# Optimization experiments

Measured on AMD Instinct MI355X. Metric: run time of the kernel, lower is better.

Reference implementation:

```python
import jax, jax.numpy as jnp
import numpy as np

D_EMBED = 1024
N_HEAD = 16
LEN_TRIM = 1024
LN_EPS = 1e-5


def setup_inputs() -> dict:
    key = jax.random.key(0)
    ks = jax.random.split(key, 8)
    B = 2
    h_q = jax.random.normal(ks[0], (B, LEN_TRIM, D_EMBED), jnp.float32)
    h_kv1 = jax.random.normal(ks[1], (B, LEN_TRIM, D_EMBED), jnp.float32)
    h_kv2 = jax.random.normal(ks[2], (B, 2 * LEN_TRIM, D_EMBED), jnp.float32)
    mask = jax.random.uniform(ks[3], (B, LEN_TRIM, 1), jnp.float32)
    in_proj_w = jax.random.normal(ks[4], (3 * D_EMBED, D_EMBED), jnp.float32) * 0.02
    in_proj_b = jnp.zeros((3 * D_EMBED,), jnp.float32)
    out_w = jax.random.normal(ks[5], (D_EMBED, D_EMBED), jnp.float32) * 0.02
    out_b = jnp.zeros((D_EMBED,), jnp.float32)
    ln_g = jnp.ones((D_EMBED,), jnp.float32)
    ln_b = jnp.zeros((D_EMBED,), jnp.float32)
    return dict(h_q=h_q, h_kv1=h_kv1, h_kv2=h_kv2, mask=mask,
                in_proj_w=in_proj_w, in_proj_b=in_proj_b,
                out_w=out_w, out_b=out_b, ln_g=ln_g, ln_b=ln_b)


def _layernorm(x, g, b):
    mu = jnp.mean(x, axis=-1, keepdims=True)
    var = jnp.mean(jnp.square(x - mu), axis=-1, keepdims=True)
    return (x - mu) * jax.lax.rsqrt(var + LN_EPS) * g + b


def reference(h_q, h_kv1, h_kv2, mask, in_proj_w, in_proj_b, out_w, out_b, ln_g, ln_b):
    B, L, D = h_q.shape
    H = N_HEAD
    dh = D // H
    h_kv = jnp.concatenate((h_kv1, h_kv2), axis=1)  # (B, 3L, D)
    S = h_kv.shape[1]
    Wq, Wk, Wv = jnp.split(in_proj_w, 3, axis=0)
    bq, bk, bv = jnp.split(in_proj_b, 3, axis=0)
    q = (h_q @ Wq.T + bq).reshape(B, L, H, dh).transpose(0, 2, 1, 3)   # (B,H,L,dh)
    k = (h_kv @ Wk.T + bk).reshape(B, S, H, dh).transpose(0, 2, 1, 3)  # (B,H,S,dh)
    v = (h_kv @ Wv.T + bv).reshape(B, S, H, dh).transpose(0, 2, 1, 3)
    scores = jnp.einsum('bhld,bhsd->bhls', q, k) / jnp.sqrt(jnp.float32(dh))
    block = jnp.triu(jnp.ones((L, L), bool), k=1)
    mask_causal = jnp.concatenate((block, block, block), axis=-1)  # (L, S)
    scores = jnp.where(mask_causal, -jnp.inf, scores)
    attn = jax.nn.softmax(scores, axis=-1)
    ctx = jnp.einsum('bhls,bhsd->bhld', attn, v).transpose(0, 2, 1, 3).reshape(B, L, D)
    attn_out = ctx @ out_w.T + out_b
    return _layernorm(h_q + attn_out, ln_g, ln_b) * mask
```

## Files before the change

### kernel.cpp

```cpp
#include <hip/hip_runtime.h>
#include <stdint.h>

typedef unsigned short u16;
typedef unsigned int u32;
typedef __bf16 bf16x8 __attribute__((ext_vector_type(8)));
typedef float floatx4 __attribute__((ext_vector_type(4)));
typedef u16 u16x8 __attribute__((ext_vector_type(8)));
typedef u16 u16x4 __attribute__((ext_vector_type(4)));

__device__ __forceinline__ u16 f2bf(float f) {
    __bf16 h = (__bf16)f;
    return __builtin_bit_cast(u16, h);
}

__device__ __forceinline__ void gll16(const u16* g, u16* l) {
    typedef __attribute__((address_space(1))) u32 gu32;
    typedef __attribute__((address_space(3))) u32 lu32;
    __builtin_amdgcn_global_load_lds((gu32*)g, (lu32*)l, 16, 0, 0);
}

__global__ __launch_bounds__(256) void cvt_all(const float* __restrict__ hq,
                                               const float* __restrict__ kv1,
                                               const float* __restrict__ kv2,
                                               const float* __restrict__ win,
                                               u16* __restrict__ a_q,
                                               u16* __restrict__ a_kv,
                                               u16* __restrict__ wb) {
    const int NQ = 262144, NKV = 786432, NW = 393216;
    int i = blockIdx.x * 256 + threadIdx.x;
    const int stride = gridDim.x * 256;
    for (; i < NQ + NKV + NW; i += stride) {
        const float* src; u16* dst;
        if (i < NQ) {
            src = hq + (long long)i * 8; dst = a_q + (long long)i * 8;
        } else if (i < NQ + NKV) {
            int c = i - NQ;
            int row = c >> 7;
            int col = (c & 127) * 8;
            int b = row >= 3072, r = row - b * 3072;
            src = (r < 1024) ? kv1 + ((long long)(b * 1024 + r)) * 1024 + col
                             : kv2 + ((long long)(b * 2048 + (r - 1024))) * 1024 + col;
            dst = a_kv + (long long)row * 1024 + col;
        } else {
            int c = i - (NQ + NKV);
            src = win + (long long)c * 8; dst = wb + (long long)c * 8;
        }
        floatx4 x = *(const floatx4*)src;
        floatx4 y = *(const floatx4*)(src + 4);
        u16x8 o;
        #pragma unroll
        for (int j = 0; j < 4; j++) { o[j] = f2bf(x[j]); o[4 + j] = f2bf(y[j]); }
        *(u16x8*)dst = o;
    }
}

__global__ __launch_bounds__(256) void cvt_bf16(const float* __restrict__ in,
                                                u16* __restrict__ out, int n8) {
    int i = blockIdx.x * 256 + threadIdx.x;
    const int stride = gridDim.x * 256;
    for (; i < n8; i += stride) {
        floatx4 a = *(const floatx4*)(in + (long long)i * 8);
        floatx4 b = *(const floatx4*)(in + (long long)i * 8 + 4);
        u16x8 o;
        #pragma unroll
        for (int j = 0; j < 4; j++) { o[j] = f2bf(a[j]); o[4 + j] = f2bf(b[j]); }
        *(u16x8*)(out + (long long)i * 8) = o;
    }
}

__global__ __launch_bounds__(256) void gemm_proj(const u16* __restrict__ aq,
                                                 const u16* __restrict__ akv,
                                                 const u16* __restrict__ wb,
                                                 const float* __restrict__ bias,
                                                 u16* __restrict__ Qo,
                                                 u16* __restrict__ Ko,
                                                 u16* __restrict__ VTg) {
    __shared__ u16 lds[2][2][8192];
    const int tid = threadIdx.x;
    const int wave = tid >> 6, lane = tid & 63;
    const int lane16 = lane & 15, quad = lane >> 4;
    const int bid = blockIdx.x;
    const int g = (bid & 7) * 112 + (bid >> 3);
    const bool qblk = g < 128;
    int my, nx;
    if (qblk) { my = g >> 3; nx = g & 7; }
    else { int gg = g - 128; my = gg >> 4; nx = gg & 15; }
    const int rowBase = my * 128;
    const int colBase = nx * 128;
    const int wrow = (qblk ? 0 : 1024) + colBase;
    const int wm = (wave >> 1) * 64, wn = (wave & 1) * 64;

    floatx4 acc[4][4];
    #pragma unroll
    for (int am = 0; am < 4; am++)
        #pragma unroll
        for (int bn = 0; bn < 4; bn++) acc[am][bn] = floatx4{0.f, 0.f, 0.f, 0.f};

    const int srow8 = tid >> 3;
    const int scol = ((tid & 7) ^ (srow8 & 7)) * 8;
    const u16* aS = (qblk ? aq : akv) + (long long)(rowBase + srow8) * 1024 + scol;
    const u16* bS = wb + (long long)(wrow + srow8) * 1024 + scol;
    u16* lbase = &lds[0][0][0];
    const int ldst = wave * 512;

    const int cko0 = ((quad ^ (lane16 & 7)) * 8);
    const int cko1 = (((4 + quad) ^ (lane16 & 7)) * 8);

    {
        u16* dA = lbase; u16* dB = lbase + 8192;
        #pragma unroll
        for (int j = 0; j < 4; j++) {
            gll16(aS + j * 32768, dA + j * 2048 + ldst);
            gll16(bS + j * 32768, dB + j * 2048 + ldst);
        }
    }
    __syncthreads();

    int buf = 0;
    for (int t = 0; t < 16; t++) {
        if (t < 15) {
            const int k0 = (t + 1) * 64;
            u16* dA = lbase + (buf ^ 1) * 16384;
            u16* dB = dA + 8192;
            #pragma unroll
            for (int j = 0; j < 4; j++) {
                gll16(aS + j * 32768 + k0, dA + j * 2048 + ldst);
                gll16(bS + j * 32768 + k0, dB + j * 2048 + ldst);
            }
        }
        const u16* Ab = lbase + buf * 16384;
        const u16* Bb = Ab + 8192;
        u16x8 a0[4], a1[4], b0[4], b1[4];
        #pragma unroll
        for (int i = 0; i < 4; i++) {
            a0[i] = *(const u16x8*)&Ab[(wm + i * 16 + lane16) * 64 + cko0];
            a1[i] = *(const u16x8*)&Ab[(wm + i * 16 + lane16) * 64 + cko1];
            b0[i] = *(const u16x8*)&Bb[(wn + i * 16 + lane16) * 64 + cko0];
            b1[i] = *(const u16x8*)&Bb[(wn + i * 16 + lane16) * 64 + cko1];
        }
        #pragma unroll
        for (int am = 0; am < 4; am++)
            #pragma unroll
            for (int bn = 0; bn < 4; bn++)
                acc[am][bn] = __builtin_amdgcn_mfma_f32_16x16x32_bf16(
                    __builtin_bit_cast(bf16x8, a0[am]),
                    __builtin_bit_cast(bf16x8, b0[bn]), acc[am][bn], 0, 0, 0);
        #pragma unroll
        for (int am = 0; am < 4; am++)
            #pragma unroll
            for (int bn = 0; bn < 4; bn++)
                acc[am][bn] = __builtin_amdgcn_mfma_f32_16x16x32_bf16(
                    __builtin_bit_cast(bf16x8, a1[am]),
                    __builtin_bit_cast(bf16x8, b1[bn]), acc[am][bn], 0, 0, 0);
        __syncthreads();
        buf ^= 1;
    }

    const float* bcol = bias + (qblk ? 0 : 1024) + colBase;
    if (qblk || nx < 8) {
        u16* Cb = qblk ? Qo : Ko;
        #pragma unroll
        for (int am = 0; am < 4; am++)
            #pragma unroll
            for (int bn = 0; bn < 4; bn++)
                #pragma unroll
                for (int r = 0; r < 4; r++) {
                    int row = rowBase + wm + am * 16 + quad * 4 + r;
                    int col = wn + bn * 16 + lane16;
                    float v = acc[am][bn][r] + bcol[col];
                    Cb[(long long)row * 1024 + colBase + col] = f2bf(v);
                }
    } else {
        const int b_ = rowBase >= 3072;
        const int keyBase = rowBase - b_ * 3072 + wm;
        #pragma unroll
        for (int am = 0; am < 4; am++)
            #pragma unroll
            for (int bn = 0; bn < 4; bn++) {
                int col = wn + bn * 16 + lane16;
                int d = colBase - 1024 + col;
                int key0 = keyBase + am * 16 + quad * 4;
                u16x4 pk;
                #pragma unroll
                for (int r = 0; r < 4; r++) pk[r] = f2bf(acc[am][bn][r] + bcol[col]);
                *(u16x4*)&VTg[((long long)(b_ * 1024 + d)) * 3072 + key0] = pk;
            }
    }
}

__global__ __launch_bounds__(256) void gemm_out(const u16* __restrict__ ctx,
                                                const u16* __restrict__ wob,
                                                const float* __restrict__ bias,
                                                float* __restrict__ ao0,
                                                float* __restrict__ ao1) {
    __shared__ u16 lds[2][2][8192];
    const int tid = threadIdx.x;
    const int wave = tid >> 6, lane = tid & 63;
    const int lane16 = lane & 15, quad = lane >> 4;
    const int bid = blockIdx.x;
    const int g = (bid & 7) * 32 + (bid >> 3);
    const int my = g >> 4;
    const int nx = (g & 15) >> 1;
    const int kh = g & 1;
    const int rowBase = my * 128, colBase = nx * 128, kbase = kh * 512;
    const int wm = (wave >> 1) * 64, wn = (wave & 1) * 64;

    floatx4 acc[4][4];
    #pragma unroll
    for (int am = 0; am < 4; am++)
        #pragma unroll
        for (int bn = 0; bn < 4; bn++) acc[am][bn] = floatx4{0.f, 0.f, 0.f, 0.f};

    const int srow8 = tid >> 3;
    const int scol = ((tid & 7) ^ (srow8 & 7)) * 8;
    const u16* aS = ctx + (long long)(rowBase + srow8) * 1024 + kbase + scol;
    const u16* bS = wob + (long long)(colBase + srow8) * 1024 + kbase + scol;
    u16* lbase = &lds[0][0][0];
    const int ldst = wave * 512;
    const int cko0 = ((quad ^ (lane16 & 7)) * 8);
    const int cko1 = (((4 + quad) ^ (lane16 & 7)) * 8);

    {
        u16* dA = lbase; u16* dB = lbase + 8192;
        #pragma unroll
        for (int j = 0; j < 4; j++) {
            gll16(aS + j * 32768, dA + j * 2048 + ldst);
            gll16(bS + j * 32768, dB + j * 2048 + ldst);
        }
    }
    __syncthreads();

    int buf = 0;
    for (int t = 0; t < 8; t++) {
        if (t < 7) {
            const int k0 = (t + 1) * 64;
            u16* dA = lbase + (buf ^ 1) * 16384;
            u16* dB = dA + 8192;
            #pragma unroll
            for (int j = 0; j < 4; j++) {
                gll16(aS + j * 32768 + k0, dA + j * 2048 + ldst);
                gll16(bS + j * 32768 + k0, dB + j * 2048 + ldst);
            }
        }
        const u16* Ab = lbase + buf * 16384;
        const u16* Bb = Ab + 8192;
        u16x8 a0[4], a1[4], b0[4], b1[4];
        #pragma unroll
        for (int i = 0; i < 4; i++) {
            a0[i] = *(const u16x8*)&Ab[(wm + i * 16 + lane16) * 64 + cko0];
            a1[i] = *(const u16x8*)&Ab[(wm + i * 16 + lane16) * 64 + cko1];
            b0[i] = *(const u16x8*)&Bb[(wn + i * 16 + lane16) * 64 + cko0];
            b1[i] = *(const u16x8*)&Bb[(wn + i * 16 + lane16) * 64 + cko1];
        }
        #pragma unroll
        for (int am = 0; am < 4; am++)
            #pragma unroll
            for (int bn = 0; bn < 4; bn++)
                acc[am][bn] = __builtin_amdgcn_mfma_f32_16x16x32_bf16(
                    __builtin_bit_cast(bf16x8, a0[am]),
                    __builtin_bit_cast(bf16x8, b0[bn]), acc[am][bn], 0, 0, 0);
        #pragma unroll
        for (int am = 0; am < 4; am++)
            #pragma unroll
            for (int bn = 0; bn < 4; bn++)
                acc[am][bn] = __builtin_amdgcn_mfma_f32_16x16x32_bf16(
                    __builtin_bit_cast(bf16x8, a1[am]),
                    __builtin_bit_cast(bf16x8, b1[bn]), acc[am][bn], 0, 0, 0);
        __syncthreads();
        buf ^= 1;
    }

    float* Co = kh ? ao1 : ao0;
    #pragma unroll
    for (int am = 0; am < 4; am++)
        #pragma unroll
        for (int bn = 0; bn < 4; bn++)
            #pragma unroll
            for (int r = 0; r < 4; r++) {
                int row = rowBase + wm + am * 16 + quad * 4 + r;
                int col = colBase + wn + bn * 16 + lane16;
                float v = acc[am][bn][r] + (kh == 0 ? bias[col] : 0.f);
                Co[(long long)row * 1024 + col] = v;
            }
}

#define ATTN_TILE(DIAG_, HAVENEXT_)                                           \
{                                                                             \
    const int cur = t & 1;                                                    \
    if (HAVENEXT_) {                                                          \
        const long long ko = (long long)(t + 1) * 65536;                      \
        const long long vo = (long long)(t + 1) * 64;                         \
        _Pragma("unroll")                                                     \
        for (int j = 0; j < 2; j++) {                                         \
            gll16(kS + ko + j * 32768, &Kt[cur ^ 1][j * 2048 + ldst]);        \
            gll16(vS + vo + (long long)j * 32 * 3072, &Vt[cur ^ 1][j * 2048 + ldst]); \
        }                                                                     \
    }                                                                         \
    floatx4 sacc[4];                                                          \
    _Pragma("unroll")                                                         \
    for (int mi = 0; mi < 4; mi++) sacc[mi] = floatx4{0.f, 0.f, 0.f, 0.f};    \
    __builtin_amdgcn_s_setprio(1);                                            \
    _Pragma("unroll")                                                         \
    for (int mi = 0; mi < 4; mi++) {                                          \
        u16x8 kf = *(const u16x8*)&Kt[cur][(mi * 16 + lane16) * 64 + slot0];  \
        sacc[mi] = __builtin_amdgcn_mfma_f32_16x16x32_bf16(                   \
            __builtin_bit_cast(bf16x8, kf), qf[0], sacc[mi], 0, 0, 0);        \
    }                                                                         \
    _Pragma("unroll")                                                         \
    for (int mi = 0; mi < 4; mi++) {                                          \
        u16x8 kf = *(const u16x8*)&Kt[cur][(mi * 16 + lane16) * 64 + slot1];  \
        sacc[mi] = __builtin_amdgcn_mfma_f32_16x16x32_bf16(                   \
            __builtin_bit_cast(bf16x8, kf), qf[1], sacc[mi], 0, 0, 0);        \
    }                                                                         \
    __builtin_amdgcn_s_setprio(0);                                            \
    float tmax = -1e30f;                                                      \
    _Pragma("unroll")                                                         \
    for (int mi = 0; mi < 4; mi++)                                            \
        _Pragma("unroll")                                                     \
        for (int r = 0; r < 4; r++) {                                         \
            float s = sacc[mi][r] * C2;                                       \
            if (DIAG_ && (mi * 16 + quad * 4 + r) > qloc) s = -1e30f;         \
            sacc[mi][r] = s;                                                  \
            tmax = fmaxf(tmax, s);                                            \
        }                                                                     \
    tmax = fmaxf(tmax, __shfl_xor(tmax, 16));                                 \
    tmax = fmaxf(tmax, __shfl_xor(tmax, 32));                                 \
    if (!__all(tmax <= m_i + 8.0f)) {           \
        float m_new = fmaxf(m_i, tmax);                                       \
        float alpha = exp2f(m_i - m_new);                                     \
        _Pragma("unroll")                                                     \
        for (int mi = 0; mi < 4; mi++)                                        \
            _Pragma("unroll")                                                 \
            for (int r = 0; r < 4; r++) o_acc[mi][r] *= alpha;                \
        l_lane *= alpha;                                                      \
        m_i = m_new;                                                          \
    }                                                                         \
    _Pragma("unroll")                                                         \
    for (int mi = 0; mi < 4; mi++) {                                          \
        u16x4 pk;                                                             \
        _Pragma("unroll")                                                     \
        for (int r = 0; r < 4; r++) {                                         \
            float p = exp2f(sacc[mi][r] - m_i);                               \
            l_lane += p;                                                      \
            pk[r] = f2bf(p);                                                  \
        }                                                                     \
        *(u16x4*)&Ps[wave][lane16 * 84 + mi * 16 + quad * 4] = pk;            \
    }                                                                         \
    __builtin_amdgcn_wave_barrier();                                          \
    __builtin_amdgcn_s_setprio(1);                                            \
    _Pragma("unroll")                                                         \
    for (int c = 0; c < 2; c++) {                                             \
        bf16x8 pf = __builtin_bit_cast(bf16x8,                                \
            *(const u16x8*)&Ps[wave][lane16 * 84 + c * 32 + quad * 8]);       \
        const int slot = c ? slot1 : slot0;                                   \
        _Pragma("unroll")                                                     \
        for (int mi = 0; mi < 4; mi++) {                                      \
            bf16x8 vf = __builtin_bit_cast(bf16x8,                            \
                *(const u16x8*)&Vt[cur][(mi * 16 + lane16) * 64 + slot]);     \
            o_acc[mi] = __builtin_amdgcn_mfma_f32_16x16x32_bf16(vf, pf, o_acc[mi], 0, 0, 0); \
        }                                                                     \
    }                                                                         \
    __builtin_amdgcn_s_setprio(0);                                            \
    if (HAVENEXT_) __syncthreads();                                           \
}

__global__ __launch_bounds__(256) void attn_seg(const u16* __restrict__ Q,
                                                const u16* __restrict__ Kb,
                                                const u16* __restrict__ VTg,
                                                float* __restrict__ pO_lo,
                                                float* __restrict__ pO_hi,
                                                float* __restrict__ pml) {
    __shared__ u16 Kt[2][4096];
    __shared__ u16 Vt[2][4096];
    __shared__ u16 Ps[4][1344];
    const int tid = threadIdx.x;
    const int wave = tid >> 6, lane = tid & 63;
    const int lane16 = lane & 15, quad = lane >> 4;
    const int bid = blockIdx.x;
    const int idx_ = (bid & 7) * 192 + (bid >> 3);
    const int qhat = idx_ & 15;
    const int h   = (idx_ >> 4) & 15;
    const int b   = (idx_ >> 8) & 1;
    const int seg = idx_ >> 9;
    const int qt = b ? (15 - qhat) : qhat;
    const int l0 = qt * 64;
    const int wq = wave * 16;
    const float C2 = 0.1803368801f;
    const int qloc = wq + lane16;

    bf16x8 qf[2];
    {
        const u16* qrow = Q + ((long long)(b * 1024 + l0 + wq + lane16)) * 1024 + h * 64;
        qf[0] = __builtin_bit_cast(bf16x8, *(const u16x8*)(qrow + quad * 8));
        qf[1] = __builtin_bit_cast(bf16x8, *(const u16x8*)(qrow + 32 + quad * 8));
    }

    const int srow = tid >> 3;
    const int csw8 = ((tid & 7) ^ (srow & 7)) * 8;
    const long long bh = ((long long)b * 3072) * 1024 + h * 64;
    const u16* kS = Kb + bh + ((long long)(seg * 1024)) * 1024
                    + (long long)srow * 1024 + csw8;
    const u16* vS = VTg + ((long long)(b * 1024 + h * 64 + srow)) * 3072
                    + seg * 1024 + csw8;
    const int ldst = wave * 512;

    {
        #pragma unroll
        for (int j = 0; j < 2; j++) {
            gll16(kS + j * 32768, &Kt[0][j * 2048 + ldst]);
            gll16(vS + (long long)j * 32 * 3072, &Vt[0][j * 2048 + ldst]);
        }
    }
    __syncthreads();

    const int slot0 = ((quad ^ (lane16 & 7)) * 8);
    const int slot1 = (((4 + quad) ^ (lane16 & 7)) * 8);

    float m_i = -1e30f, l_lane = 0.f;
    floatx4 o_acc[4];
    #pragma unroll
    for (int mi = 0; mi < 4; mi++) o_acc[mi] = floatx4{0.f, 0.f, 0.f, 0.f};

    for (int t = 0; t < qt; t++) ATTN_TILE(false, true)
    { int t = qt; ATTN_TILE(true, false) }

    float l_i = l_lane;
    l_i += __shfl_xor(l_i, 16);
    l_i += __shfl_xor(l_i, 32);

    const int p = ((b * 16 + h) * 16 + qt) * 3 + seg;
    float* op = (p < 512) ? (pO_lo + (long long)p * 4096)
                          : (pO_hi + (long long)(p - 512) * 4096);
    if (quad == 0) {
        pml[(long long)p * 128 + (wq + lane16) * 2]     = m_i;
        pml[(long long)p * 128 + (wq + lane16) * 2 + 1] = l_i;
    }
    float* orow = op + (long long)(wq + lane16) * 64;
    #pragma unroll
    for (int mi = 0; mi < 4; mi++)
        *(floatx4*)(orow + mi * 16 + quad * 4) = o_acc[mi];
}

__global__ __launch_bounds__(256) void attn_combine(const float* __restrict__ pO_lo,
                                                    const float* __restrict__ pO_hi,
                                                    const float* __restrict__ pml,
                                                    u16* __restrict__ Ctx) {
    const int g = blockIdx.x;
    const int qt = g & 15;
    const int h  = (g >> 4) & 15;
    const int b  = g >> 8;
    const int t  = threadIdx.x;
    const int q  = t >> 2;
    const int d0 = (t & 3) * 16;
    const int p0 = g * 3;

    float m[3], l[3];
    #pragma unroll
    for (int s = 0; s < 3; s++) {
        m[s] = pml[(long long)(p0 + s) * 128 + q * 2];
        l[s] = pml[(long long)(p0 + s) * 128 + q * 2 + 1];
    }
    float M = fmaxf(m[0], fmaxf(m[1], m[2]));
    float w[3];
    #pragma unroll
    for (int s = 0; s < 3; s++) w[s] = exp2f(m[s] - M);
    float L = w[0] * l[0] + w[1] * l[1] + w[2] * l[2];
    float invL = 1.0f / L;

    const float* O[3];
    #pragma unroll
    for (int s = 0; s < 3; s++) {
        int pp = p0 + s;
        O[s] = ((pp < 512) ? (pO_lo + (long long)pp * 4096)
                           : (pO_hi + (long long)(pp - 512) * 4096))
               + (long long)q * 64 + d0;
    }

    long long crow = ((long long)(b * 1024 + qt * 64 + q)) * 1024 + h * 64 + d0;
    #pragma unroll
    for (int i = 0; i < 16; i += 4) {
        floatx4 a  = *(const floatx4*)(O[0] + i);
        floatx4 bb = *(const floatx4*)(O[1] + i);
        floatx4 cc = *(const floatx4*)(O[2] + i);
        #pragma unroll
        for (int j = 0; j < 4; j++)
            Ctx[crow + i + j] = f2bf((w[0] * a[j] + w[1] * bb[j] + w[2] * cc[j]) * invL);
    }
}

__global__ __launch_bounds__(256) void ln_kernel(const float* __restrict__ AO0,
                                                 const float* __restrict__ AO1,
                                                 const float* __restrict__ HQ,
                                                 const float* __restrict__ g,
                                                 const float* __restrict__ bb,
                                                 const float* __restrict__ mask,
                                                 float* __restrict__ Out) {
    const int row = blockIdx.x;
    const int t = threadIdx.x;
    const int base = row * 1024 + t * 4;
    floatx4 a0 = *(const floatx4*)&AO0[base];
    floatx4 a1 = *(const floatx4*)&AO1[base];
    floatx4 hq = *(const floatx4*)&HQ[base];
    float x[4];
    #pragma unroll
    for (int i = 0; i < 4; i++) x[i] = a0[i] + a1[i] + hq[i];
    float s = x[0] + x[1] + x[2] + x[3];
    float ss = x[0]*x[0] + x[1]*x[1] + x[2]*x[2] + x[3]*x[3];
    #pragma unroll
    for (int off = 32; off >= 1; off >>= 1) { s += __shfl_xor(s, off); ss += __shfl_xor(ss, off); }
    __shared__ float smem[8];
    int wave = t >> 6, lane = t & 63;
    if (lane == 0) { smem[wave] = s; smem[4 + wave] = ss; }
    __syncthreads();
    s  = smem[0] + smem[1] + smem[2] + smem[3];
    ss = smem[4] + smem[5] + smem[6] + smem[7];
    float mu  = s * (1.f / 1024.f);
    float var = ss * (1.f / 1024.f) - mu * mu;
    float rs  = rsqrtf(var + 1e-5f);
    float mv  = mask[row];
    floatx4 g4 = *(const floatx4*)&g[t * 4];
    floatx4 b4 = *(const floatx4*)&bb[t * 4];
    floatx4 y4;
    #pragma unroll
    for (int i = 0; i < 4; i++) y4[i] = ((x[i] - mu) * rs * g4[i] + b4[i]) * mv;
    *(floatx4*)&Out[base] = y4;
}

extern "C" void kernel_launch(void* const* d_in, const int* in_sizes, int n_in,
                              void* d_out, int out_size, void* d_ws, size_t ws_size,
                              hipStream_t stream) {
    (void)in_sizes; (void)n_in; (void)out_size; (void)ws_size;
    const float* h_q   = (const float*)d_in[0];
    const float* h_kv1 = (const float*)d_in[1];
    const float* h_kv2 = (const float*)d_in[2];
    const float* maskp = (const float*)d_in[3];
    const float* win   = (const float*)d_in[4];
    const float* binp  = (const float*)d_in[5];
    const float* wout  = (const float*)d_in[6];
    const float* bout  = (const float*)d_in[7];
    const float* ln_g  = (const float*)d_in[8];
    const float* ln_b  = (const float*)d_in[9];
    float* outp = (float*)d_out;

    char* ws = (char*)d_ws;
    const size_t MB = 1024 * 1024;
    u16*   q_b   = (u16*)(ws);
    u16*   k_b   = (u16*)(ws + 4 * MB);
    u16*   vT    = (u16*)(ws + 16 * MB);
    u16*   ctx_b = q_b;
    u16*   a_q   = (u16*)(ws + 28 * MB);
    u16*   a_kv  = (u16*)(ws + 32 * MB);
    u16*   wb    = (u16*)d_out;
    float* pO_lo = (float*)d_out;
    float* pO_hi = (float*)(ws + 28 * MB);
    u16*   wob   = (u16*)(ws + 28 * MB);
    float* pml   = (float*)(ws + 44 * MB);
    float* ao0   = (float*)(ws + 4 * MB);
    float* ao1   = (float*)(ws + 12 * MB);

    cvt_all<<<2048, 256, 0, stream>>>(h_q, h_kv1, h_kv2, win, a_q, a_kv, wb);
    gemm_proj<<<896, 256, 0, stream>>>(a_q, a_kv, wb, binp, q_b, k_b, vT);
    attn_seg<<<1536, 256, 0, stream>>>(q_b, k_b, vT, pO_lo, pO_hi, pml);
    attn_combine<<<512, 256, 0, stream>>>(pO_lo, pO_hi, pml, ctx_b);
    cvt_bf16<<<512, 256, 0, stream>>>(wout, wob, 131072);
    gemm_out<<<256, 256, 0, stream>>>(ctx_b, wob, bout, ao0, ao1);
    ln_kernel<<<2048, 256, 0, stream>>>(ao0, ao1, h_q, ln_g, ln_b, maskp, outp);
}
```

Baseline: 225.9 us.

## Fold softmax scale into Q projection, relax attention waits, and swizzle P tile

```diff
diff --git a/kernel.cpp b/kernel.cpp
--- a/kernel.cpp
+++ b/kernel.cpp
@@ -168,6 +168,7 @@
                     int row = rowBase + wm + am * 16 + quad * 4 + r;
                     int col = wn + bn * 16 + lane16;
                     float v = acc[am][bn][r] + bcol[col];
+                    if (qblk) v *= 0.1803368801f;
                     Cb[(long long)row * 1024 + colBase + col] = f2bf(v);
                 }
     } else {
@@ -295,7 +296,11 @@
             gll16(kS + ko + j * 32768, &Kt[cur ^ 1][j * 2048 + ldst]);        \
             gll16(vS + vo + (long long)j * 32 * 3072, &Vt[cur ^ 1][j * 2048 + ldst]); \
         }                                                                     \
-    }                                                                         \
+        asm volatile("s_waitcnt vmcnt(4)" ::: "memory");   \
+    } else {                                                                  \
+        asm volatile("s_waitcnt vmcnt(0)" ::: "memory");                      \
+    }                                                                         \
+    __builtin_amdgcn_sched_barrier(0);                                        \
     floatx4 sacc[4];                                                          \
     _Pragma("unroll")                                                         \
     for (int mi = 0; mi < 4; mi++) sacc[mi] = floatx4{0.f, 0.f, 0.f, 0.f};    \
@@ -313,20 +318,24 @@
             __builtin_bit_cast(bf16x8, kf), qf[1], sacc[mi], 0, 0, 0);        \
     }                                                                         \
     __builtin_amdgcn_s_setprio(0);                                            \
-    float tmax = -1e30f;                                                      \
+    if (DIAG_) {                                \
+        _Pragma("unroll")                                                     \
+        for (int mi = 0; mi < 4; mi++)                                        \
+            _Pragma("unroll")                                                 \
+            for (int r = 0; r < 4; r++)                                       \
+                if ((mi * 16 + quad * 4 + r) > qloc) sacc[mi][r] = -1e30f;    \
+    }                                                                         \
+    float tmax = fmaxf(sacc[0][0], sacc[0][1]);       \
+    tmax = fmaxf(tmax, fmaxf(sacc[0][2], sacc[0][3]));                        \
     _Pragma("unroll")                                                         \
-    for (int mi = 0; mi < 4; mi++)                                            \
-        _Pragma("unroll")                                                     \
-        for (int r = 0; r < 4; r++) {                                         \
-            float s = sacc[mi][r] * C2;                                       \
-            if (DIAG_ && (mi * 16 + quad * 4 + r) > qloc) s = -1e30f;         \
-            sacc[mi][r] = s;                                                  \
-            tmax = fmaxf(tmax, s);                                            \
-        }                                                                     \
-    tmax = fmaxf(tmax, __shfl_xor(tmax, 16));                                 \
-    tmax = fmaxf(tmax, __shfl_xor(tmax, 32));                                 \
+    for (int mi = 1; mi < 4; mi++) {                                          \
+        tmax = fmaxf(tmax, fmaxf(sacc[mi][0], sacc[mi][1]));                  \
+        tmax = fmaxf(tmax, fmaxf(sacc[mi][2], sacc[mi][3]));                  \
+    }                                                                         \
     if (!__all(tmax <= m_i + 8.0f)) {           \
-        float m_new = fmaxf(m_i, tmax);                                       \
+        float tr = fmaxf(tmax, __shfl_xor(tmax, 16));                         \
+        tr = fmaxf(tr, __shfl_xor(tr, 32));                                   \
+        float m_new = fmaxf(m_i, tr);                                         \
         float alpha = exp2f(m_i - m_new);                                     \
         _Pragma("unroll")                                                     \
         for (int mi = 0; mi < 4; mi++)                                        \
@@ -344,14 +353,15 @@
             l_lane += p;                                                      \
             pk[r] = f2bf(p);                                                  \
         }                                                                     \
-        *(u16x4*)&Ps[wave][lane16 * 84 + mi * 16 + quad * 4] = pk;            \
+        *(u16x4*)&Ps[wave][lane16 * 64 +                                      \
+            (((mi * 2 + (quad >> 1)) ^ (lane16 & 7)) << 3) + (quad & 1) * 4] = pk; \
     }                                                                         \
     __builtin_amdgcn_wave_barrier();                                          \
     __builtin_amdgcn_s_setprio(1);                                            \
     _Pragma("unroll")                                                         \
     for (int c = 0; c < 2; c++) {                                             \
-        bf16x8 pf = __builtin_bit_cast(bf16x8,                                \
-            *(const u16x8*)&Ps[wave][lane16 * 84 + c * 32 + quad * 8]);       \
+        bf16x8 pf = __builtin_bit_cast(bf16x8, *(const u16x8*)&Ps[wave][      \
+            lane16 * 64 + (((c * 4 + quad) ^ (lane16 & 7)) << 3)]);           \
         const int slot = c ? slot1 : slot0;                                   \
         _Pragma("unroll")                                                     \
         for (int mi = 0; mi < 4; mi++) {                                      \
@@ -361,7 +371,11 @@
         }                                                                     \
     }                                                                         \
     __builtin_amdgcn_s_setprio(0);                                            \
-    if (HAVENEXT_) __syncthreads();                                           \
+    if (HAVENEXT_) {                            \
+        asm volatile("s_waitcnt lgkmcnt(0)" ::: "memory");                    \
+        __builtin_amdgcn_s_barrier();                                         \
+        __builtin_amdgcn_sched_barrier(0);                                    \
+    }                                                                         \
 }
 
 __global__ __launch_bounds__(256) void attn_seg(const u16* __restrict__ Q,
@@ -372,7 +386,7 @@
                                                 float* __restrict__ pml) {
     __shared__ u16 Kt[2][4096];
     __shared__ u16 Vt[2][4096];
-    __shared__ u16 Ps[4][1344];
+    __shared__ u16 Ps[4][1024];
     const int tid = threadIdx.x;
     const int wave = tid >> 6, lane = tid & 63;
     const int lane16 = lane & 15, quad = lane >> 4;
@@ -385,7 +399,6 @@
     const int qt = b ? (15 - qhat) : qhat;
     const int l0 = qt * 64;
     const int wq = wave * 16;
-    const float C2 = 0.1803368801f;
     const int qloc = wq + lane16;
 
     bf16x8 qf[2];
```

New measurement: 225.9 us. Within noise of the previous version (+0.0%).
